# Kernel optimization log

Hardware: AMD Instinct MI355X
Metric: run time of the kernel (lower is better)

Reference implementation:

```python
import jax, jax.numpy as jnp
import numpy as np

# Module constants (from init_kwargs)
SR = 16000
HOP_LENGTH = 256
HOP_MS = 40
WIN_LENGTHS = (80, 160)
MARGIN = 0.2
SPOOF_WEIGHT = 0.5
MEL_SAMPLE = 16
MAX_TIME_WINDOWS = 64
SEED = 123
EPS = 1e-12  # F.normalize default eps


def _ms_to_frames(ms):
    samples = int(SR * (ms / 1000.0))
    return max(3, samples // HOP_LENGTH)


def _window_starts(T, w_frames, hop_frames):
    # Replicates _frames() + linspace capping (all static, done in numpy).
    starts = np.arange(0, T - w_frames + 1, hop_frames, dtype=np.int64)
    if starts.size == 0:
        return np.zeros((1,), dtype=np.int64), T
    if MAX_TIME_WINDOWS and starts.size > MAX_TIME_WINDOWS:
        sel = np.linspace(0, starts.size - 1, MAX_TIME_WINDOWS).astype(np.int64)
        starts = starts[sel]
    return starts, w_frames


def _mel_indices(M):
    if MEL_SAMPLE and MEL_SAMPLE < M:
        return np.random.default_rng(SEED).permutation(M)[:MEL_SAMPLE]
    return np.arange(M)


def _head(x, W1, W2):
    # 1x1 convs (no bias) == per-pixel channel GEMMs.  x: [B,C,M,T]
    h = jax.nn.relu(jnp.einsum('bcmt,oc->bomt', x, W1))
    return jnp.einsum('bcmt,oc->bomt', h, W2)


def _cosine_distance(u, v):
    un = u / jnp.maximum(jnp.linalg.norm(u, axis=-1, keepdims=True), EPS)
    vn = v / jnp.maximum(jnp.linalg.norm(v, axis=-1, keepdims=True), EPS)
    return 1.0 - (un * vn).sum(axis=-1)


def _windowed_dists(A_sel, P_sel, starts, w):
    # A_sel, P_sel: [B, C, Ms, T]; gather all windows at once.
    B, C, Ms, T = A_sel.shape
    nW = starts.shape[0]
    idx = jnp.asarray(starts[:, None] + np.arange(w)[None, :]).ravel()  # [nW*w]
    u = jnp.take(A_sel, idx, axis=3).reshape(B, C, Ms, nW, w)
    v = jnp.take(P_sel, idx, axis=3).reshape(B, C, Ms, nW, w)
    # flatten (C, w) per window -> feature dim (dot/norm are order-invariant)
    u = jnp.moveaxis(u, 1, 3).reshape(B, Ms, nW, C * w)
    v = jnp.moveaxis(v, 1, 3).reshape(B, Ms, nW, C * w)
    return _cosine_distance(u, v).reshape(B, Ms * nW)  # [B, Ms*nW]


def _forward(A_map, P_map, y, W1a, W2a, W1p, W2p):
    B, _, M, T = A_map.shape
    A_loc = _head(A_map, W1a, W2a)
    P_loc = _head(P_map, W1p, W2p)
    idx_m = _mel_indices(M)
    A_sel = A_loc[:, :, idx_m, :]
    P_sel = P_loc[:, :, idx_m, :]
    hop_frames = _ms_to_frames(HOP_MS)

    dists = []
    for w_ms in WIN_LENGTHS:
        w = _ms_to_frames(w_ms)
        starts, w_eff = _window_starts(T, w, hop_frames)
        dists.append(_windowed_dists(A_sel, P_sel, starts, w_eff))
    D = jnp.concatenate(dists, axis=1)  # [B, n_total_windows]

    mask_r = (y == 0)
    mask_s = (y == 1)
    nr = mask_r.sum()
    ns = mask_s.sum()
    mr = mask_r.astype(D.dtype)
    ms_ = mask_s.astype(D.dtype)
    # per-window mean over real samples, then mean over windows (== sum/count)
    real_mean = (D * mr[:, None]).sum(axis=0) / jnp.maximum(nr, 1).astype(D.dtype)
    spoof_mean = (jax.nn.relu(MARGIN - D) * ms_[:, None]).sum(axis=0) / jnp.maximum(ns, 1).astype(D.dtype)
    loss_real = jnp.where(nr > 0, real_mean.mean(), jnp.array(0.0, D.dtype))
    loss_spoof = jnp.where(ns > 0, spoof_mean.mean(), jnp.array(0.0, D.dtype))
    stc_loss = loss_real + SPOOF_WEIGHT * loss_spoof  # tv_weight = 0
    coh_score = 1.0 - D.mean(axis=1)  # [B]
    return stc_loss, coh_score


def setup_inputs() -> dict:
    key = jax.random.key(0)
    k = jax.random.split(key, 8)
    B, M, T = 32, 80, 2000
    return {
        'A_map': jax.random.normal(k[0], (B, 1, M, T), dtype=jnp.float32),
        'P_map': jax.random.normal(k[1], (B, 1, M, T), dtype=jnp.float32),
        'y': jax.random.randint(k[2], (B,), 0, 2, dtype=jnp.int32),
        'W1a': jax.random.normal(k[3], (8, 1), dtype=jnp.float32) * 0.5,
        'W2a': jax.random.normal(k[4], (8, 8), dtype=jnp.float32) * 0.25,
        'W1p': jax.random.normal(k[5], (8, 1), dtype=jnp.float32) * 0.5,
        'W2p': jax.random.normal(k[6], (8, 8), dtype=jnp.float32) * 0.25,
    }


def reference(A_map, P_map, y, W1a, W2a, W1p, W2p):
    return _forward(A_map, P_map, y, W1a, W2a, W1p, W2p)
```

## Files before the change

### kernel.cpp

```cpp
#include <hip/hip_runtime.h>
#include <stdint.h>

#define NB 32
#define NM 80
#define NT 2000
#define MSEL 16
#define NWIN 128
#define NBLK (NB * MSEL)
#define NCOLS 2048.0f

struct Params {
    int mel[MSEL];
    int start[NWIN];
};

__device__ float2 g_part[NBLK];

template <int W>
__device__ inline void win_acc(const float* __restrict__ sA,
                               const float* __restrict__ sP,
                               int s, float4 c0, float4 c1,
                               float& dot, float& na, float& npv)
{
    #pragma unroll
    for (int t = 0; t < W; ++t) {
        float a = sA[s + t];
        float p = sP[s + t];
        float k  = (a >= 0.f) ? ((p >= 0.f) ? c0.w : c0.z)
                              : ((p >= 0.f) ? c0.y : c0.x);
        float sa = (a >= 0.f) ? c1.y : c1.x;
        float sp = (p >= 0.f) ? c1.w : c1.z;
        dot += a * p * k;
        na  += a * a * sa;
        npv += p * p * sp;
    }
}

__global__ __launch_bounds__(128) void asn_win_kernel(
    const float* __restrict__ A, const float* __restrict__ P,
    const float* __restrict__ W1a, const float* __restrict__ W2a,
    const float* __restrict__ W1p, const float* __restrict__ W2p,
    Params prm)
{
    __shared__ float4 sA4[NT / 4];
    __shared__ float4 sP4[NT / 4];
    __shared__ float4 sCoefV[2];
    __shared__ float  wsum[2][2];

    const float* sA = (const float*)sA4;
    const float* sP = (const float*)sP4;

    const int blk = blockIdx.x;
    const int b   = blk >> 4;
    const int msi = blk & 15;
    const int m   = prm.mel[msi];
    const int tid = threadIdx.x;

    const float4* arow = (const float4*)(A + ((size_t)b * NM + m) * NT);
    const float4* prow = (const float4*)(P + ((size_t)b * NM + m) * NT);

    if (tid < 64) {
        const int c = tid & 7;
        float w2a = W2a[tid];
        float w2p = W2p[tid];
        float w1a_l = (tid < 8) ? W1a[tid] : 0.f;
        float w1p_l = (tid < 8) ? W1p[tid] : 0.f;
        float wa = __shfl(w1a_l, c);
        float wp = __shfl(w1p_l, c);

        float ta = wa * w2a, tp = wp * w2p;
        float cap = (wa > 0.f) ? ta : 0.f;
        float can = (wa < 0.f) ? ta : 0.f;
        float cqp = (wp > 0.f) ? tp : 0.f;
        float cqn = (wp < 0.f) ? tp : 0.f;

        #pragma unroll
        for (int off = 1; off < 8; off <<= 1) {
            cap += __shfl_xor(cap, off);
            can += __shfl_xor(can, off);
            cqp += __shfl_xor(cqp, off);
            cqn += __shfl_xor(cqn, off);
        }

        const bool rep = (c == 0);
        float q0 = rep ? can * cqn : 0.f;
        float q1 = rep ? can * cqp : 0.f;
        float q2 = rep ? cap * cqn : 0.f;
        float q3 = rep ? cap * cqp : 0.f;
        float q4 = rep ? can * can : 0.f;
        float q5 = rep ? cap * cap : 0.f;
        float q6 = rep ? cqn * cqn : 0.f;
        float q7 = rep ? cqp * cqp : 0.f;
        #pragma unroll
        for (int off = 8; off < 64; off <<= 1) {
            q0 += __shfl_xor(q0, off);
            q1 += __shfl_xor(q1, off);
            q2 += __shfl_xor(q2, off);
            q3 += __shfl_xor(q3, off);
            q4 += __shfl_xor(q4, off);
            q5 += __shfl_xor(q5, off);
            q6 += __shfl_xor(q6, off);
            q7 += __shfl_xor(q7, off);
        }
        if (tid == 0) {
            sCoefV[0] = make_float4(q0, q1, q2, q3);
            sCoefV[1] = make_float4(q4, q5, q6, q7);
        }
    }

    {
        const int  t0 = tid, t1 = tid + 128, t2 = tid + 256, t3 = tid + 384;
        const bool g3 = (t3 < NT / 4);
        float4 a0 = arow[t0], p0 = prow[t0];
        float4 a1 = arow[t1], p1 = prow[t1];
        float4 a2 = arow[t2], p2 = prow[t2];
        float4 a3, p3;
        if (g3) { a3 = arow[t3]; p3 = prow[t3]; }
        sA4[t0] = a0;  sP4[t0] = p0;
        sA4[t1] = a1;  sP4[t1] = p1;
        sA4[t2] = a2;  sP4[t2] = p2;
        if (g3) { sA4[t3] = a3;  sP4[t3] = p3; }
    }

    __syncthreads();

    const float4 c0 = sCoefV[0];
    const float4 c1 = sCoefV[1];

    const int s = prm.start[tid];
    float dot = 0.f, na = 0.f, npv = 0.f;
    if (tid < 64) win_acc<5> (sA, sP, s, c0, c1, dot, na, npv);
    else          win_acc<10>(sA, sP, s, c0, c1, dot, na, npv);

    float nu = fmaxf(sqrtf(na),  1e-12f);
    float nv = fmaxf(sqrtf(npv), 1e-12f);
    float dist = 1.f - dot / (nu * nv);
    float rd   = fmaxf(0.2f - dist, 0.f);

    float s1 = dist, s2 = rd;
    #pragma unroll
    for (int off = 32; off; off >>= 1) {
        s1 += __shfl_down(s1, off);
        s2 += __shfl_down(s2, off);
    }
    if ((tid & 63) == 0) {
        wsum[tid >> 6][0] = s1;
        wsum[tid >> 6][1] = s2;
    }
    __syncthreads();
    if (tid == 0) {
        g_part[blk] = make_float2(wsum[0][0] + wsum[1][0],
                                  wsum[0][1] + wsum[1][1]);
    }
}

__global__ __launch_bounds__(64) void asn_final_kernel(
    const int* __restrict__ y, float* __restrict__ out)
{
    const int tid = threadIdx.x;

    float aR = 0.f, aS = 0.f;
    float colsum[8];
    #pragma unroll
    for (int r = 0; r < 8; ++r) {
        int k  = r * 64 + tid;
        int bb = k >> 4;
        float2 v = g_part[k];
        if (y[bb] == 0) aR += v.x; else aS += v.y;
        colsum[r] = v.x;
    }
    #pragma unroll
    for (int off = 32; off; off >>= 1) {
        aR += __shfl_down(aR, off);
        aS += __shfl_down(aS, off);
    }

    #pragma unroll
    for (int r = 0; r < 8; ++r) {
        float v = colsum[r];
        #pragma unroll
        for (int off = 8; off; off >>= 1) v += __shfl_down(v, off);
        if ((tid & 15) == 0) {
            int bb = r * 4 + (tid >> 4);
            out[1 + bb] = 1.f - v * (1.0f / NCOLS);
        }
    }

    if (tid == 0) {
        int nr = 0, ns = 0;
        for (int bb = 0; bb < NB; ++bb) { int yb = y[bb]; nr += (yb == 0); ns += (yb == 1); }
        float lr = aR / (NCOLS * (float)(nr > 0 ? nr : 1));
        float ls = aS / (NCOLS * (float)(ns > 0 ? ns : 1));
        out[0] = lr + 0.5f * ls;
    }
}

static void compute_params(Params& prm)
{
    const uint32_t INIT_A = 0x43b0d7e5u, MULT_A = 0x931e8875u;
    const uint32_t INIT_B = 0x8b51f9ddu, MULT_B = 0x58f38dedu;

    uint32_t hc = INIT_A;
    auto hashmix = [&](uint32_t v) -> uint32_t {
        v ^= hc; hc *= MULT_A; v *= hc; v ^= v >> 16; return v;
    };
    auto mix = [](uint32_t x, uint32_t y) -> uint32_t {
        uint32_t r = (x * 0xca01f9ddu) ^ (y * 0x4973f715u);
        r ^= r >> 16; return r;
    };

    uint32_t pool[4];
    const uint32_t entropy[1] = { 123u };
    for (int i = 0; i < 4; ++i) pool[i] = hashmix(i < 1 ? entropy[i] : 0u);
    for (int s = 0; s < 4; ++s)
        for (int d = 0; d < 4; ++d)
            if (s != d) pool[d] = mix(pool[d], hashmix(pool[s]));

    uint32_t w32[8];
    uint32_t hc2 = INIT_B;
    for (int i = 0; i < 8; ++i) {
        uint32_t v = pool[i & 3];
        v ^= hc2; hc2 *= MULT_B; v *= hc2; v ^= v >> 16;
        w32[i] = v;
    }
    uint64_t sd[4];
    for (int i = 0; i < 4; ++i)
        sd[i] = (uint64_t)w32[2 * i] | ((uint64_t)w32[2 * i + 1] << 32);

    typedef __uint128_t u128;
    const u128 MULT = ((u128)0x2360ed051fc65da4ULL << 64) | 0x4385df649fccf645ULL;
    u128 initstate = ((u128)sd[0] << 64) | sd[1];
    u128 initseq   = ((u128)sd[2] << 64) | sd[3];
    u128 state = 0, inc = (initseq << 1) | 1;
    state = state * MULT + inc;
    state += initstate;
    state = state * MULT + inc;

    bool has32 = false; uint32_t buf32 = 0;
    auto next64 = [&]() -> uint64_t {
        state = state * MULT + inc;
        uint64_t hi = (uint64_t)(state >> 64);
        uint64_t lo = (uint64_t)state;
        uint64_t x = hi ^ lo;
        unsigned rot = (unsigned)(state >> 122);
        return (x >> rot) | (x << ((64u - rot) & 63u));
    };
    auto next32 = [&]() -> uint32_t {
        if (has32) { has32 = false; return buf32; }
        uint64_t v = next64();
        has32 = true; buf32 = (uint32_t)(v >> 32);
        return (uint32_t)v;
    };

    int perm[NM];
    for (int i = 0; i < NM; ++i) perm[i] = i;
    for (int i = NM - 1; i >= 1; --i) {
        uint32_t mask = (uint32_t)i;
        mask |= mask >> 1; mask |= mask >> 2; mask |= mask >> 4;
        mask |= mask >> 8; mask |= mask >> 16;
        uint32_t j;
        do { j = next32() & mask; } while (j > (uint32_t)i);
        int tmp = perm[i]; perm[i] = perm[(int)j]; perm[(int)j] = tmp;
    }
    for (int i = 0; i < MSEL; ++i) prm.mel[i] = perm[i];

    {
        const double step = 665.0 / 63.0;
        for (int i = 0; i < 64; ++i) {
            long long sel = (i == 63) ? 665LL : (long long)((double)i * step);
            prm.start[i] = (int)(3LL * sel);
        }
    }
    {
        const double step = 663.0 / 63.0;
        for (int i = 0; i < 64; ++i) {
            long long sel = (i == 63) ? 663LL : (long long)((double)i * step);
            prm.start[64 + i] = (int)(3LL * sel);
        }
    }
}

extern "C" void kernel_launch(void* const* d_in, const int* in_sizes, int n_in,
                              void* d_out, int out_size, void* d_ws, size_t ws_size,
                              hipStream_t stream)
{
    const float* A   = (const float*)d_in[0];
    const float* P   = (const float*)d_in[1];
    const int*   y   = (const int*)d_in[2];
    const float* W1a = (const float*)d_in[3];
    const float* W2a = (const float*)d_in[4];
    const float* W1p = (const float*)d_in[5];
    const float* W2p = (const float*)d_in[6];
    float* out = (float*)d_out;
    (void)d_ws; (void)ws_size;

    Params prm;
    compute_params(prm);

    asn_win_kernel<<<dim3(NBLK), dim3(128), 0, stream>>>(
        A, P, W1a, W2a, W1p, W2p, prm);
    asn_final_kernel<<<dim3(1), dim3(64), 0, stream>>>(y, out);
}
```

Baseline: 94.82 us.

## Gather window samples directly from global memory instead of staging rows in LDS

Drops the shared-memory staging of the full 2000-sample A/P rows. Each thread now loads only its own window samples straight from global memory, which cuts the full-row reads down to just the windowed spans. Every wave computes the coefficients redundantly, and per-wave partial sums are written to a float4 slot that the final kernel combines, so both __syncthreads are gone. The trade-off is uncoalesced scalar global loads, where overlapping windows depend on the cache.

New measurement: 94.12 us. No clear change (-0.7%).

```diff
diff --git a/kernel.cpp b/kernel.cpp
--- a/kernel.cpp
+++ b/kernel.cpp
@@ -14,18 +14,21 @@
     int start[NWIN];
 };
 
-__device__ float2 g_part[NBLK];
+__device__ float4 g_part4[NBLK];
 
 template <int W>
-__device__ inline void win_acc(const float* __restrict__ sA,
-                               const float* __restrict__ sP,
-                               int s, float4 c0, float4 c1,
-                               float& dot, float& na, float& npv)
-{
+__device__ inline void win_gather(const float* __restrict__ arow,
+                                  const float* __restrict__ prow,
+                                  int s, float4 c0, float4 c1,
+                                  float& dot, float& na, float& npv)
+{
+    float av[W], pv[W];
+    #pragma unroll
+    for (int t = 0; t < W; ++t) { av[t] = arow[s + t]; pv[t] = prow[s + t]; }
     #pragma unroll
     for (int t = 0; t < W; ++t) {
-        float a = sA[s + t];
-        float p = sP[s + t];
+        float a = av[t];
+        float p = pv[t];
         float k  = (a >= 0.f) ? ((p >= 0.f) ? c0.w : c0.z)
                               : ((p >= 0.f) ? c0.y : c0.x);
         float sa = (a >= 0.f) ? c1.y : c1.x;
@@ -42,95 +45,68 @@
     const float* __restrict__ W1p, const float* __restrict__ W2p,
     Params prm)
 {
-    __shared__ float4 sA4[NT / 4];
-    __shared__ float4 sP4[NT / 4];
-    __shared__ float4 sCoefV[2];
-    __shared__ float  wsum[2][2];
-
-    const float* sA = (const float*)sA4;
-    const float* sP = (const float*)sP4;
-
-    const int blk = blockIdx.x;
-    const int b   = blk >> 4;
-    const int msi = blk & 15;
-    const int m   = prm.mel[msi];
-    const int tid = threadIdx.x;
-
-    const float4* arow = (const float4*)(A + ((size_t)b * NM + m) * NT);
-    const float4* prow = (const float4*)(P + ((size_t)b * NM + m) * NT);
-
-    if (tid < 64) {
-        const int c = tid & 7;
-        float w2a = W2a[tid];
-        float w2p = W2p[tid];
-        float w1a_l = (tid < 8) ? W1a[tid] : 0.f;
-        float w1p_l = (tid < 8) ? W1p[tid] : 0.f;
-        float wa = __shfl(w1a_l, c);
-        float wp = __shfl(w1p_l, c);
-
-        float ta = wa * w2a, tp = wp * w2p;
-        float cap = (wa > 0.f) ? ta : 0.f;
-        float can = (wa < 0.f) ? ta : 0.f;
-        float cqp = (wp > 0.f) ? tp : 0.f;
-        float cqn = (wp < 0.f) ? tp : 0.f;
-
-        #pragma unroll
-        for (int off = 1; off < 8; off <<= 1) {
-            cap += __shfl_xor(cap, off);
-            can += __shfl_xor(can, off);
-            cqp += __shfl_xor(cqp, off);
-            cqn += __shfl_xor(cqn, off);
-        }
-
-        const bool rep = (c == 0);
-        float q0 = rep ? can * cqn : 0.f;
-        float q1 = rep ? can * cqp : 0.f;
-        float q2 = rep ? cap * cqn : 0.f;
-        float q3 = rep ? cap * cqp : 0.f;
-        float q4 = rep ? can * can : 0.f;
-        float q5 = rep ? cap * cap : 0.f;
-        float q6 = rep ? cqn * cqn : 0.f;
-        float q7 = rep ? cqp * cqp : 0.f;
-        #pragma unroll
-        for (int off = 8; off < 64; off <<= 1) {
-            q0 += __shfl_xor(q0, off);
-            q1 += __shfl_xor(q1, off);
-            q2 += __shfl_xor(q2, off);
-            q3 += __shfl_xor(q3, off);
-            q4 += __shfl_xor(q4, off);
-            q5 += __shfl_xor(q5, off);
-            q6 += __shfl_xor(q6, off);
-            q7 += __shfl_xor(q7, off);
-        }
-        if (tid == 0) {
-            sCoefV[0] = make_float4(q0, q1, q2, q3);
-            sCoefV[1] = make_float4(q4, q5, q6, q7);
-        }
-    }
-
-    {
-        const int  t0 = tid, t1 = tid + 128, t2 = tid + 256, t3 = tid + 384;
-        const bool g3 = (t3 < NT / 4);
-        float4 a0 = arow[t0], p0 = prow[t0];
-        float4 a1 = arow[t1], p1 = prow[t1];
-        float4 a2 = arow[t2], p2 = prow[t2];
-        float4 a3, p3;
-        if (g3) { a3 = arow[t3]; p3 = prow[t3]; }
-        sA4[t0] = a0;  sP4[t0] = p0;
-        sA4[t1] = a1;  sP4[t1] = p1;
-        sA4[t2] = a2;  sP4[t2] = p2;
-        if (g3) { sA4[t3] = a3;  sP4[t3] = p3; }
-    }
-
-    __syncthreads();
-
-    const float4 c0 = sCoefV[0];
-    const float4 c1 = sCoefV[1];
+    const int blk  = blockIdx.x;
+    const int b    = blk >> 4;
+    const int msi  = blk & 15;
+    const int m    = prm.mel[msi];
+    const int tid  = threadIdx.x;
+    const int wv   = tid >> 6;
+    const int lane = tid & 63;
+
+    const float* arow = A + ((size_t)b * NM + m) * NT;
+    const float* prow = P + ((size_t)b * NM + m) * NT;
+
+    const int c = lane & 7;
+    float w2a = W2a[lane];
+    float w2p = W2p[lane];
+    float w1a_l = (lane < 8) ? W1a[lane] : 0.f;
+    float w1p_l = (lane < 8) ? W1p[lane] : 0.f;
+    float wa = __shfl(w1a_l, c);
+    float wp = __shfl(w1p_l, c);
+
+    float ta = wa * w2a, tp = wp * w2p;
+    float cap = (wa > 0.f) ? ta : 0.f;
+    float can = (wa < 0.f) ? ta : 0.f;
+    float cqp = (wp > 0.f) ? tp : 0.f;
+    float cqn = (wp < 0.f) ? tp : 0.f;
+
+    #pragma unroll
+    for (int off = 1; off < 8; off <<= 1) {
+        cap += __shfl_xor(cap, off);
+        can += __shfl_xor(can, off);
+        cqp += __shfl_xor(cqp, off);
+        cqn += __shfl_xor(cqn, off);
+    }
+
+    const bool rep = (c == 0);
+    float q0 = rep ? can * cqn : 0.f;
+    float q1 = rep ? can * cqp : 0.f;
+    float q2 = rep ? cap * cqn : 0.f;
+    float q3 = rep ? cap * cqp : 0.f;
+    float q4 = rep ? can * can : 0.f;
+    float q5 = rep ? cap * cap : 0.f;
+    float q6 = rep ? cqn * cqn : 0.f;
+    float q7 = rep ? cqp * cqp : 0.f;
+    #pragma unroll
+    for (int off = 8; off < 64; off <<= 1) {
+        q0 += __shfl_xor(q0, off);
+        q1 += __shfl_xor(q1, off);
+        q2 += __shfl_xor(q2, off);
+        q3 += __shfl_xor(q3, off);
+        q4 += __shfl_xor(q4, off);
+        q5 += __shfl_xor(q5, off);
+        q6 += __shfl_xor(q6, off);
+        q7 += __shfl_xor(q7, off);
+    }
+    q0 = __shfl(q0, 0); q1 = __shfl(q1, 0); q2 = __shfl(q2, 0); q3 = __shfl(q3, 0);
+    q4 = __shfl(q4, 0); q5 = __shfl(q5, 0); q6 = __shfl(q6, 0); q7 = __shfl(q7, 0);
+    const float4 c0 = make_float4(q0, q1, q2, q3);
+    const float4 c1 = make_float4(q4, q5, q6, q7);
 
     const int s = prm.start[tid];
     float dot = 0.f, na = 0.f, npv = 0.f;
-    if (tid < 64) win_acc<5> (sA, sP, s, c0, c1, dot, na, npv);
-    else          win_acc<10>(sA, sP, s, c0, c1, dot, na, npv);
+    if (wv == 0) win_gather<5> (arow, prow, s, c0, c1, dot, na, npv);
+    else         win_gather<10>(arow, prow, s, c0, c1, dot, na, npv);
 
     float nu = fmaxf(sqrtf(na),  1e-12f);
     float nv = fmaxf(sqrtf(npv), 1e-12f);
@@ -143,14 +119,8 @@
         s1 += __shfl_down(s1, off);
         s2 += __shfl_down(s2, off);
     }
-    if ((tid & 63) == 0) {
-        wsum[tid >> 6][0] = s1;
-        wsum[tid >> 6][1] = s2;
-    }
-    __syncthreads();
-    if (tid == 0) {
-        g_part[blk] = make_float2(wsum[0][0] + wsum[1][0],
-                                  wsum[0][1] + wsum[1][1]);
+    if (lane == 0) {
+        ((float2*)&g_part4[blk])[wv] = make_float2(s1, s2);
     }
 }
 
@@ -165,9 +135,11 @@
     for (int r = 0; r < 8; ++r) {
         int k  = r * 64 + tid;
         int bb = k >> 4;
-        float2 v = g_part[k];
-        if (y[bb] == 0) aR += v.x; else aS += v.y;
-        colsum[r] = v.x;
+        float4 q = g_part4[k];
+        float d  = q.x + q.z;
+        float sv = q.y + q.w;
+        if (y[bb] == 0) aR += d; else aS += sv;
+        colsum[r] = d;
     }
     #pragma unroll
     for (int off = 32; off; off >>= 1) {
```
